# Kernel optimization log

Hardware: AMD Instinct MI355X
Metric: run time of the kernel (lower is better)

## Reference

```python
import jax, jax.numpy as jnp
import numpy as np

H = 8          # head_num
DK = 16        # qkv_dim
CLIP = 10.0    # logit clipping


def _heads(x):
    # (b, n, H*DK) -> (b, H, n, DK)
    b, n, _ = x.shape
    return x.reshape(b, n, H, DK).transpose(0, 2, 1, 3)


def setup_inputs() -> dict:
    key = jax.random.key(0)
    ks = jax.random.split(key, 10)
    batch, problem, d, klen = 2048, 100, 128, 10
    s = 1.0 / np.sqrt(d)
    problems = jax.random.uniform(ks[0], (batch, problem, 2), dtype=jnp.float32)
    encoded_nodes = jax.random.normal(ks[1], (batch, problem, d), dtype=jnp.float32)
    Wq_first = jax.random.normal(ks[2], (d, H * DK), dtype=jnp.float32) * s
    Wq_last = jax.random.normal(ks[3], (d, H * DK), dtype=jnp.float32) * s
    Wk = jax.random.normal(ks[4], (d, H * DK), dtype=jnp.float32) * s
    Wv = jax.random.normal(ks[5], (d, H * DK), dtype=jnp.float32) * s
    Wcomb = jax.random.normal(ks[6], (H * DK, d), dtype=jnp.float32) * s
    # prefix: k distinct node indices per batch row (first k of a random permutation)
    perm = jax.vmap(lambda kk: jax.random.permutation(kk, problem))(
        jax.random.split(ks[7], batch))
    prefix = perm[:, :klen].astype(jnp.int32)
    return {"problems": problems, "encoded_nodes": encoded_nodes,
            "Wq_first": Wq_first, "Wq_last": Wq_last, "Wk": Wk, "Wv": Wv,
            "Wcomb": Wcomb, "prefix": prefix}


def reference(problems, encoded_nodes, Wq_first, Wq_last, Wk, Wv, Wcomb, prefix):
    batch, problem, d = encoded_nodes.shape
    b_idx = jnp.arange(batch)
    sqrt_dk = jnp.sqrt(jnp.float32(DK))
    sqrt_d = jnp.sqrt(jnp.float32(d))

    # set_kv: precompute multi-head K, V once (single-head key = encoded_nodes)
    kh = _heads(encoded_nodes @ Wk)   # (b, H, n, DK)
    vh = _heads(encoded_nodes @ Wv)   # (b, H, n, DK)

    # set_q1: query contribution of the first node (last node of prefix)
    last0 = prefix[:, -1]
    q1 = _heads(encoded_nodes[b_idx, last0][:, None, :] @ Wq_first)  # (b, H, 1, DK)

    # visited mask from prefix
    visited0 = jnp.zeros((batch, problem), dtype=bool)
    visited0 = visited0.at[b_idx[:, None], prefix].set(True)

    def step(carry, _):
        visited, cur = carry
        enc_last = encoded_nodes[b_idx, cur][:, None, :]            # (b, 1, d)
        q = q1 + _heads(enc_last @ Wq_last)                         # (b, H, 1, DK)
        ninf = jnp.where(visited, -jnp.inf, 0.0)                    # (b, n)
        scores = jnp.einsum('bhqe,bhne->bhqn', q, kh) / sqrt_dk
        att = jax.nn.softmax(scores + ninf[:, None, None, :], axis=-1)
        mh = jnp.einsum('bhqn,bhne->bhqe', att, vh)                 # (b, H, 1, DK)
        mh = mh.transpose(0, 2, 1, 3).reshape(batch, 1, H * DK) @ Wcomb  # (b, 1, d)
        sc = jnp.einsum('bqd,bnd->bqn', mh, encoded_nodes)[:, 0] / sqrt_d  # (b, n)
        logits = CLIP * jnp.tanh(sc) + ninf
        sel = jnp.argmax(logits, axis=-1)                           # (b,)
        visited = visited.at[b_idx, sel].set(True)
        return (visited, sel), sel

    steps = problem - prefix.shape[1]
    _, sels = jax.lax.scan(step, (visited0, last0), None, length=steps)
    tour = jnp.concatenate([prefix, sels.T.astype(prefix.dtype)], axis=1)  # (b, problem)
    return tour
```

## Files before the change

### kernel.cpp

```cpp
#include <hip/hip_runtime.h>
#include <math.h>

#define N      100
#define D      128
#define KL     10
#define S0     90
#define STEPS  90
#define LDK    132
#define NT     512

__device__ __forceinline__ float dot4(float4 a, float4 b) {
  return a.x*b.x + a.y*b.y + a.z*b.z + a.w*b.w;
}
__device__ __forceinline__ void fma4(float4& acc, float a, float4 v) {
  acc.x += a*v.x; acc.y += a*v.y; acc.z += a*v.z; acc.w += a*v.w;
}

template<int RPT>
__device__ __forceinline__ void cc(const float* __restrict__ encB,
                                   const float* __restrict__ W,
                                   bool wRowMajor, int base, int cnt,
                                   const int* __restrict__ slotNode,
                                   float* __restrict__ stage, int tid) {
  const int col = tid & 127;
  const int grp = tid >> 7;
  float acc[RPT];
  int   nd [RPT];
  #pragma unroll
  for (int ii = 0; ii < RPT; ++ii) {
    acc[ii] = 0.f;
    int r = grp + 4*ii;
    nd[ii] = (r < cnt) ? __builtin_amdgcn_readfirstlane(slotNode[base + r]) : 0;
  }
  for (int dd = 0; dd < D; dd += 16) {
    float w[16];
    #pragma unroll
    for (int t = 0; t < 16; ++t)
      w[t] = wRowMajor ? W[col*D + dd + t] : W[(dd+t)*D + col];
    #pragma unroll
    for (int ii = 0; ii < RPT; ++ii) {
      int r = grp + 4*ii;
      if (r < cnt) {
        const float* er = encB + (size_t)nd[ii]*D + dd;
        float a0=0,a1=0,a2=0,a3=0;
        #pragma unroll
        for (int t = 0; t < 16; t += 4) {
          a0 += er[t]*w[t];   a1 += er[t+1]*w[t+1];
          a2 += er[t+2]*w[t+2]; a3 += er[t+3]*w[t+3];
        }
        acc[ii] += (a0+a1)+(a2+a3);
      }
    }
  }
  #pragma unroll
  for (int ii = 0; ii < RPT; ++ii) {
    int r = grp + 4*ii;
    if (r < cnt) stage[(base + r)*LDK + col] = acc[ii];
  }
}

__global__ __launch_bounds__(NT, 4)
void policy_kernel(const float* __restrict__ enc,
                   const float* __restrict__ Wq_first,
                   const float* __restrict__ Wq_last,
                   const float* __restrict__ Wk,
                   const float* __restrict__ Wv,
                   const float* __restrict__ Wcomb,
                   const int*   __restrict__ prefix,
                   int*         __restrict__ out) {
  __shared__ __align__(16) float sCE[S0*LDK];
  __shared__ __align__(16) float sq[D];
  __shared__ __align__(16) float sMh[D];
  __shared__ float sSum[8];
  __shared__ int   sSlotNode[96];
  __shared__ unsigned long long sPacked[2];
  __shared__ int   sLast0;

  const int tid = threadIdx.x;
  const int b   = blockIdx.x;
  const float* encB = enc + (size_t)b*N*D;

  if (tid < KL) out[(size_t)b*N + tid] = prefix[b*KL + tid];
  if (tid == 0) {
    unsigned vis[4] = {0u,0u,0u,0u};
    const int* pr = prefix + b*KL;
    for (int j = 0; j < KL; ++j) { int n = pr[j]; vis[n>>5] |= 1u << (n&31); }
    int cnt = 0;
    for (int n = 0; n < N; ++n)
      if (!((vis[n>>5] >> (n&31)) & 1u)) sSlotNode[cnt++] = n;
    sLast0 = pr[KL-1];
    sPacked[0] = 0ull; sPacked[1] = 0ull;
  }
  __syncthreads();

  if (tid < D) {
    const int last0 = sLast0;
    const float* er = encB + (size_t)last0*D;
    float a0=0,a1=0,a2=0,a3=0;
    #pragma unroll
    for (int d = 0; d < D; d += 4) {
      a0 += er[d]  *Wq_first[d*D     + tid];
      a1 += er[d+1]*Wq_first[(d+1)*D + tid];
      a2 += er[d+2]*Wq_first[(d+2)*D + tid];
      a3 += er[d+3]*Wq_first[(d+3)*D + tid];
    }
    sMh[tid] = (a0+a1)+(a2+a3);
  }
  __syncthreads();

  const int h = tid >> 6, l = tid & 63;

  {
    const int col = tid & 127;
    const int grp = tid >> 7;
    float acc[23]; int nd[23];
    #pragma unroll
    for (int ii = 0; ii < 23; ++ii) {
      int r = grp + 4*ii;
      acc[ii] = 0.f;
      nd[ii] = (r < S0) ? __builtin_amdgcn_readfirstlane(sSlotNode[r])
                        : ((r == S0) ? sLast0 : 0);
    }
    for (int dd = 0; dd < D; dd += 16) {
      float w[16];
      #pragma unroll
      for (int t = 0; t < 16; ++t) w[t] = Wq_last[(dd+t)*D + col];
      #pragma unroll
      for (int ii = 0; ii < 23; ++ii) {
        int r = grp + 4*ii;
        if (r <= S0) {
          const float* er = encB + (size_t)nd[ii]*D + dd;
          float a0=0,a1=0,a2=0,a3=0;
          #pragma unroll
          for (int t = 0; t < 16; t += 4) {
            a0 += er[t]*w[t];   a1 += er[t+1]*w[t+1];
            a2 += er[t+2]*w[t+2]; a3 += er[t+3]*w[t+3];
          }
          acc[ii] += (a0+a1)+(a2+a3);
        }
      }
    }
    #pragma unroll
    for (int ii = 0; ii < 23; ++ii) {
      int r = grp + 4*ii;
      if (r < S0)       sCE[r*LDK + col] = acc[ii];
      else if (r == S0) sq[col] = acc[ii] + sMh[col];
    }
  }
  __syncthreads();

  const int qcol = (h << 4) | (l & 15);
  const int qrg  = l >> 4;
  float qp[23];
  {
    const float q1c = sMh[qcol];
    #pragma unroll
    for (int ii = 0; ii < 23; ++ii) {
      int r = qrg + 4*ii;
      qp[ii] = (r < S0) ? (sCE[r*LDK + qcol] + q1c) : 0.f;
    }
  }
  __syncthreads();

  cc<23>(encB, Wk, false, 0, S0, sSlotNode, sCE, tid);
  __syncthreads();
  float4 ka0,ka1,ka2,ka3, kb0,kb1,kb2,kb3;
  {
    const float* p = &sCE[l*LDK + h*16];
    ka0 = *(const float4*)(p+0);  ka1 = *(const float4*)(p+4);
    ka2 = *(const float4*)(p+8);  ka3 = *(const float4*)(p+12);
  }
  if (l < 26) {
    const float* p = &sCE[(64+l)*LDK + h*16];
    kb0 = *(const float4*)(p+0);  kb1 = *(const float4*)(p+4);
    kb2 = *(const float4*)(p+8);  kb3 = *(const float4*)(p+12);
  } else {
    kb0=kb1=kb2=kb3 = make_float4(0.f,0.f,0.f,0.f);
  }
  __syncthreads();

  const int cQuad = tid >> 4;
  const int cStrm = tid & 15;
  const int ch    = cQuad >> 2;
  cc<12>(encB, Wv, false,  0, 48, sSlotNode, sCE, tid);
  cc<12>(encB, Wv, false, 48, 42, sSlotNode, sCE, tid);
  __syncthreads();
  float4 v0,v1,v2,v3,v4,v5;
  v0 = *(const float4*)&sCE[(cStrm     )*LDK + cQuad*4];
  v1 = *(const float4*)&sCE[(cStrm + 16)*LDK + cQuad*4];
  v2 = *(const float4*)&sCE[(cStrm + 32)*LDK + cQuad*4];
  v3 = *(const float4*)&sCE[(cStrm + 48)*LDK + cQuad*4];
  v4 = *(const float4*)&sCE[(cStrm + 64)*LDK + cQuad*4];
  v5 = (cStrm < 10) ? *(const float4*)&sCE[(cStrm + 80)*LDK + cQuad*4]
                    : make_float4(0.f,0.f,0.f,0.f);
  __syncthreads();

  cc<6>(encB, Wcomb, true,  0, 24, sSlotNode, sCE, tid);
  cc<6>(encB, Wcomb, true, 24, 24, sSlotNode, sCE, tid);
  cc<6>(encB, Wcomb, true, 48, 24, sSlotNode, sCE, tid);
  cc<6>(encB, Wcomb, true, 72, 18, sSlotNode, sCE, tid);
  __syncthreads();

  const int di  = tid >> 2;
  const int dkc = tid & 3;
  float visA = 0.f, visB = 0.f, visD = 0.f;

  for (int step = 0; step < STEPS; ++step) {
    float x0, x1;
    {
      const float4 q0 = *(const float4*)&sq[h*16 + 0];
      const float4 q1 = *(const float4*)&sq[h*16 + 4];
      const float4 q2 = *(const float4*)&sq[h*16 + 8];
      const float4 q3 = *(const float4*)&sq[h*16 + 12];
      float s0 = dot4(q0,ka0)+dot4(q1,ka1)+dot4(q2,ka2)+dot4(q3,ka3);
      x0 = expf(s0*0.25f + visA);
      x1 = 0.f;
      if (l < 26) {
        float s1 = dot4(q0,kb0)+dot4(q1,kb1)+dot4(q2,kb2)+dot4(q3,kb3);
        x1 = expf(s1*0.25f + visB);
      }
      float loc = x0 + x1;
      #pragma unroll
      for (int off = 32; off; off >>= 1) loc += __shfl_xor(loc, off);
      if (l == 0) sSum[h] = loc;
    }

    {
      const float a0 = __shfl(x0, cStrm);
      const float a1 = __shfl(x0, cStrm + 16);
      const float a2 = __shfl(x0, cStrm + 32);
      const float a3 = __shfl(x0, cStrm + 48);
      const float a4 = __shfl(x1, cStrm);
      const float a5 = __shfl(x1, cStrm + 16);
      float4 acc = make_float4(0.f,0.f,0.f,0.f);
      fma4(acc, a0, v0);
      fma4(acc, a1, v1);
      fma4(acc, a2, v2);
      fma4(acc, a3, v3);
      fma4(acc, a4, v4);
      fma4(acc, a5, v5);
      #pragma unroll
      for (int off = 1; off < 16; off <<= 1) {
        acc.x += __shfl_xor(acc.x, off);
        acc.y += __shfl_xor(acc.y, off);
        acc.z += __shfl_xor(acc.z, off);
        acc.w += __shfl_xor(acc.w, off);
      }
      if (cStrm == 0) {
        const float r = 1.0f / sSum[ch];
        float4 o; o.x=acc.x*r; o.y=acc.y*r; o.z=acc.z*r; o.w=acc.w*r;
        *(float4*)&sMh[cQuad*4] = o;
      }
    }
    __syncthreads();

    if (tid == NT-1) sPacked[(step+1)&1] = 0ull;

    if (tid < 384) {
      float a = 0.f;
      #pragma unroll
      for (int j = 0; j < 8; ++j) {
        const float4 ce = *(const float4*)&sCE[di*LDK + dkc*32 + j*4];
        const float4 mh = *(const float4*)&sMh[dkc*32 + j*4];
        a += dot4(ce, mh);
      }
      a += __shfl_xor(a, 1);
      a += __shfl_xor(a, 2);
      float val = (di < S0) ? a + visD : -INFINITY;
      int   idx = (di < S0) ? di : 127;
      #pragma unroll
      for (int off = 4; off <= 32; off <<= 1) {
        float ov = __shfl_xor(val, off);
        int   oi = __shfl_xor(idx, off);
        if (ov > val || (ov == val && oi < idx)) { val = ov; idx = oi; }
      }
      if (l == 0) {
        unsigned s = __float_as_uint(val);
        s = (s & 0x80000000u) ? ~s : (s | 0x80000000u);
        unsigned long long pk = ((unsigned long long)s << 32)
                              | (unsigned long long)(unsigned)(127 - idx);
        atomicMax(&sPacked[step&1], pk);
      }
    }
    __syncthreads();

    {
      const unsigned long long u = sPacked[step & 1];
      const int idx = __builtin_amdgcn_readfirstlane(127 - (int)(u & 0xFFull));
      if (tid == 0) out[(size_t)b*N + KL + step] = sSlotNode[idx];
      if (idx == l)      visA = -INFINITY;
      if (idx == l + 64) visB = -INFINITY;
      if (idx == di)     visD = -INFINITY;
      const int want = idx >> 2;
      float qv = qp[0];
      #pragma unroll
      for (int ii = 1; ii < 23; ++ii) qv = (want == ii) ? qp[ii] : qv;
      if (qrg == (idx & 3)) sq[qcol] = qv;
    }
  }
}

extern "C" void kernel_launch(void* const* d_in, const int* in_sizes, int n_in,
                              void* d_out, int out_size, void* d_ws, size_t ws_size,
                              hipStream_t stream) {
  const float* enc      = (const float*)d_in[1];
  const float* Wq_first = (const float*)d_in[2];
  const float* Wq_last  = (const float*)d_in[3];
  const float* Wk       = (const float*)d_in[4];
  const float* Wv       = (const float*)d_in[5];
  const float* Wcomb    = (const float*)d_in[6];
  const int*   prefix   = (const int*)d_in[7];
  const int batch = in_sizes[7] / KL;
  policy_kernel<<<batch, NT, 0, stream>>>(enc, Wq_first, Wq_last, Wk, Wv, Wcomb,
                                          prefix, (int*)d_out);
}
```

Baseline: 2.520 ms.

## Split per-node projections into a separate wide GEMM kernel via workspace

Moves the K, V, Wcomb and Wq_last projections of all 100 nodes into a separate setup kernel that uses 52 blocks per batch row and writes results to a global workspace. The decode kernel then gathers the 90 unvisited rows from the workspace into shared memory instead of computing the projections inside one 512-thread block per batch row. This exposes far more parallelism for the projection phase. In exchange it adds a round-trip of about 200 KB per batch row through global memory, computes the 10 prefix rows it does not need, and adds a second launch. It falls back to the fused kernel when the workspace is too small.

```diff
diff --git a/kernel.cpp b/kernel.cpp
--- a/kernel.cpp
+++ b/kernel.cpp
@@ -9,11 +9,77 @@
 #define LDK    132
 #define NT     512
 
+#define WS_PER_KIND 12800
+#define WS_PER_B    51200
+
 __device__ __forceinline__ float dot4(float4 a, float4 b) {
   return a.x*b.x + a.y*b.y + a.z*b.z + a.w*b.w;
 }
 __device__ __forceinline__ void fma4(float4& acc, float a, float4 v) {
   acc.x += a*v.x; acc.y += a*v.y; acc.z += a*v.z; acc.w += a*v.w;
+}
+
+__global__ __launch_bounds__(256)
+void setup_gemm(const float* __restrict__ enc,
+                const float* __restrict__ Wk,
+                const float* __restrict__ Wv,
+                const float* __restrict__ Wcomb,
+                const float* __restrict__ Wq_last,
+                float* __restrict__ ws) {
+  const int blk  = blockIdx.x;
+  const int rem  = blk % 52;
+  const int b    = blk / 52;
+  const int kind = rem / 13;
+  const int tile = rem % 13;
+  const int col  = threadIdx.x & 127;
+  const int rh   = threadIdx.x >> 7;
+  const float* W = (kind==0) ? Wk : (kind==1) ? Wv : (kind==2) ? Wcomb : Wq_last;
+  const bool rowMajor = (kind == 2);
+  const float* encB = enc + (size_t)b*N*D;
+
+  int rows[4];
+  float acc[4];
+  #pragma unroll
+  for (int j = 0; j < 4; ++j) { rows[j] = tile*8 + rh + 2*j; acc[j] = 0.f; }
+
+  for (int dd = 0; dd < D; dd += 16) {
+    float w[16];
+    #pragma unroll
+    for (int t = 0; t < 16; ++t)
+      w[t] = rowMajor ? W[col*D + dd + t] : W[(dd+t)*D + col];
+    #pragma unroll
+    for (int j = 0; j < 4; ++j) {
+      if (rows[j] < N) {
+        const float* er = encB + (size_t)rows[j]*D + dd;
+        float a0=0,a1=0,a2=0,a3=0;
+        #pragma unroll
+        for (int t = 0; t < 16; t += 4) {
+          a0 += er[t]*w[t];   a1 += er[t+1]*w[t+1];
+          a2 += er[t+2]*w[t+2]; a3 += er[t+3]*w[t+3];
+        }
+        acc[j] += (a0+a1)+(a2+a3);
+      }
+    }
+  }
+  float* o = ws + ((size_t)b*4 + kind)*WS_PER_KIND;
+  #pragma unroll
+  for (int j = 0; j < 4; ++j)
+    if (rows[j] < N) o[rows[j]*D + col] = acc[j];
+}
+
+__device__ __forceinline__ void stage90(const float* __restrict__ wsKind,
+                                        const int* __restrict__ slotNode,
+                                        float* __restrict__ sCE, int tid) {
+  const int c4  = (tid & 31) * 4;
+  const int grp = tid >> 5;
+  #pragma unroll
+  for (int ii = 0; ii < 6; ++ii) {
+    int r = grp + 16*ii;
+    if (r < S0) {
+      int nd = slotNode[r];
+      *(float4*)&sCE[r*LDK + c4] = *(const float4*)&wsKind[(size_t)nd*D + c4];
+    }
+  }
 }
 
 template<int RPT>
@@ -57,6 +123,228 @@
     int r = grp + 4*ii;
     if (r < cnt) stage[(base + r)*LDK + col] = acc[ii];
   }
+}
+
+struct DecodeState {
+  float4 ka0,ka1,ka2,ka3, kb0,kb1,kb2,kb3;
+  float4 v0,v1,v2,v3,v4,v5;
+  float  qp[23];
+};
+
+__device__ __forceinline__ void decode_loop(DecodeState& st,
+                                            float* sq, float* sMh, float* sSum,
+                                            float* sCE, int* sSlotNode,
+                                            unsigned long long* sPacked,
+                                            int tid, int b,
+                                            int* __restrict__ out) {
+  const int h = tid >> 6, l = tid & 63;
+  const int qcol = (h << 4) | (l & 15);
+  const int qrg  = l >> 4;
+  const int cQuad = tid >> 4;
+  const int cStrm = tid & 15;
+  const int ch    = cQuad >> 2;
+  const int di  = tid >> 2;
+  const int dkc = tid & 3;
+  float visA = 0.f, visB = 0.f, visD = 0.f;
+
+  for (int step = 0; step < STEPS; ++step) {
+    float x0, x1;
+    {
+      const float4 q0 = *(const float4*)&sq[h*16 + 0];
+      const float4 q1 = *(const float4*)&sq[h*16 + 4];
+      const float4 q2 = *(const float4*)&sq[h*16 + 8];
+      const float4 q3 = *(const float4*)&sq[h*16 + 12];
+      float s0 = dot4(q0,st.ka0)+dot4(q1,st.ka1)+dot4(q2,st.ka2)+dot4(q3,st.ka3);
+      x0 = expf(s0*0.25f + visA);
+      x1 = 0.f;
+      if (l < 26) {
+        float s1 = dot4(q0,st.kb0)+dot4(q1,st.kb1)+dot4(q2,st.kb2)+dot4(q3,st.kb3);
+        x1 = expf(s1*0.25f + visB);
+      }
+      float loc = x0 + x1;
+      #pragma unroll
+      for (int off = 32; off; off >>= 1) loc += __shfl_xor(loc, off);
+      if (l == 0) sSum[h] = loc;
+    }
+
+    {
+      const float a0 = __shfl(x0, cStrm);
+      const float a1 = __shfl(x0, cStrm + 16);
+      const float a2 = __shfl(x0, cStrm + 32);
+      const float a3 = __shfl(x0, cStrm + 48);
+      const float a4 = __shfl(x1, cStrm);
+      const float a5 = __shfl(x1, cStrm + 16);
+      float4 acc = make_float4(0.f,0.f,0.f,0.f);
+      fma4(acc, a0, st.v0);
+      fma4(acc, a1, st.v1);
+      fma4(acc, a2, st.v2);
+      fma4(acc, a3, st.v3);
+      fma4(acc, a4, st.v4);
+      fma4(acc, a5, st.v5);
+      #pragma unroll
+      for (int off = 1; off < 16; off <<= 1) {
+        acc.x += __shfl_xor(acc.x, off);
+        acc.y += __shfl_xor(acc.y, off);
+        acc.z += __shfl_xor(acc.z, off);
+        acc.w += __shfl_xor(acc.w, off);
+      }
+      if (cStrm == 0) {
+        const float r = 1.0f / sSum[ch];
+        float4 o; o.x=acc.x*r; o.y=acc.y*r; o.z=acc.z*r; o.w=acc.w*r;
+        *(float4*)&sMh[cQuad*4] = o;
+      }
+    }
+    __syncthreads();
+
+    if (tid == NT-1) sPacked[(step+1)&1] = 0ull;
+
+    if (tid < 384) {
+      float a = 0.f;
+      #pragma unroll
+      for (int j = 0; j < 8; ++j) {
+        const float4 ce = *(const float4*)&sCE[di*LDK + dkc*32 + j*4];
+        const float4 mh = *(const float4*)&sMh[dkc*32 + j*4];
+        a += dot4(ce, mh);
+      }
+      a += __shfl_xor(a, 1);
+      a += __shfl_xor(a, 2);
+      float val = (di < S0) ? a + visD : -INFINITY;
+      int   idx = (di < S0) ? di : 127;
+      #pragma unroll
+      for (int off = 4; off <= 32; off <<= 1) {
+        float ov = __shfl_xor(val, off);
+        int   oi = __shfl_xor(idx, off);
+        if (ov > val || (ov == val && oi < idx)) { val = ov; idx = oi; }
+      }
+      if (l == 0) {
+        unsigned s = __float_as_uint(val);
+        s = (s & 0x80000000u) ? ~s : (s | 0x80000000u);
+        unsigned long long pk = ((unsigned long long)s << 32)
+                              | (unsigned long long)(unsigned)(127 - idx);
+        atomicMax(&sPacked[step&1], pk);
+      }
+    }
+    __syncthreads();
+
+    {
+      const unsigned long long u = sPacked[step & 1];
+      const int idx = __builtin_amdgcn_readfirstlane(127 - (int)(u & 0xFFull));
+      if (tid == 0) out[(size_t)b*N + KL + step] = sSlotNode[idx];
+      if (idx == l)      visA = -INFINITY;
+      if (idx == l + 64) visB = -INFINITY;
+      if (idx == di)     visD = -INFINITY;
+      const int want = idx >> 2;
+      float qv = st.qp[0];
+      #pragma unroll
+      for (int ii = 1; ii < 23; ++ii) qv = (want == ii) ? st.qp[ii] : qv;
+      if (qrg == (idx & 3)) sq[qcol] = qv;
+    }
+  }
+}
+
+__global__ __launch_bounds__(NT, 4)
+void policy_kernel_split(const float* __restrict__ enc,
+                         const float* __restrict__ Wq_first,
+                         const int*   __restrict__ prefix,
+                         const float* __restrict__ ws,
+                         int*         __restrict__ out) {
+  __shared__ __align__(16) float sCE[S0*LDK];
+  __shared__ __align__(16) float sq[D];
+  __shared__ __align__(16) float sMh[D];
+  __shared__ float sSum[8];
+  __shared__ int   sSlotNode[96];
+  __shared__ unsigned long long sPacked[2];
+  __shared__ int   sLast0;
+
+  const int tid = threadIdx.x;
+  const int b   = blockIdx.x;
+  const float* encB = enc + (size_t)b*N*D;
+  const float* wsB  = ws + (size_t)b*WS_PER_B;
+  const float* wsK  = wsB;
+  const float* wsV  = wsB + WS_PER_KIND;
+  const float* wsCE = wsB + 2*WS_PER_KIND;
+  const float* wsQ  = wsB + 3*WS_PER_KIND;
+
+  if (tid < KL) out[(size_t)b*N + tid] = prefix[b*KL + tid];
+  if (tid == 0) {
+    unsigned vis[4] = {0u,0u,0u,0u};
+    const int* pr = prefix + b*KL;
+    for (int j = 0; j < KL; ++j) { int n = pr[j]; vis[n>>5] |= 1u << (n&31); }
+    int cnt = 0;
+    for (int n = 0; n < N; ++n)
+      if (!((vis[n>>5] >> (n&31)) & 1u)) sSlotNode[cnt++] = n;
+    sLast0 = pr[KL-1];
+    sPacked[0] = 0ull; sPacked[1] = 0ull;
+  }
+  __syncthreads();
+
+  if (tid < D) {
+    const int last0 = sLast0;
+    const float* er = encB + (size_t)last0*D;
+    float a0=0,a1=0,a2=0,a3=0;
+    #pragma unroll
+    for (int d = 0; d < D; d += 4) {
+      a0 += er[d]  *Wq_first[d*D     + tid];
+      a1 += er[d+1]*Wq_first[(d+1)*D + tid];
+      a2 += er[d+2]*Wq_first[(d+2)*D + tid];
+      a3 += er[d+3]*Wq_first[(d+3)*D + tid];
+    }
+    sMh[tid] = (a0+a1)+(a2+a3);
+  }
+  __syncthreads();
+
+  const int h = tid >> 6, l = tid & 63;
+  const int qcol = (h << 4) | (l & 15);
+  const int qrg  = l >> 4;
+  DecodeState st;
+
+  stage90(wsQ, sSlotNode, sCE, tid);
+  if (tid < D) sq[tid] = wsQ[(size_t)sLast0*D + tid] + sMh[tid];
+  __syncthreads();
+
+  {
+    const float q1c = sMh[qcol];
+    #pragma unroll
+    for (int ii = 0; ii < 23; ++ii) {
+      int r = qrg + 4*ii;
+      st.qp[ii] = (r < S0) ? (sCE[r*LDK + qcol] + q1c) : 0.f;
+    }
+  }
+  __syncthreads();
+
+  stage90(wsK, sSlotNode, sCE, tid);
+  __syncthreads();
+  {
+    const float* p = &sCE[l*LDK + h*16];
+    st.ka0 = *(const float4*)(p+0);  st.ka1 = *(const float4*)(p+4);
+    st.ka2 = *(const float4*)(p+8);  st.ka3 = *(const float4*)(p+12);
+  }
+  if (l < 26) {
+    const float* p = &sCE[(64+l)*LDK + h*16];
+    st.kb0 = *(const float4*)(p+0);  st.kb1 = *(const float4*)(p+4);
+    st.kb2 = *(const float4*)(p+8);  st.kb3 = *(const float4*)(p+12);
+  } else {
+    st.kb0=st.kb1=st.kb2=st.kb3 = make_float4(0.f,0.f,0.f,0.f);
+  }
+  __syncthreads();
+
+  const int cQuad = tid >> 4;
+  const int cStrm = tid & 15;
+  stage90(wsV, sSlotNode, sCE, tid);
+  __syncthreads();
+  st.v0 = *(const float4*)&sCE[(cStrm     )*LDK + cQuad*4];
+  st.v1 = *(const float4*)&sCE[(cStrm + 16)*LDK + cQuad*4];
+  st.v2 = *(const float4*)&sCE[(cStrm + 32)*LDK + cQuad*4];
+  st.v3 = *(const float4*)&sCE[(cStrm + 48)*LDK + cQuad*4];
+  st.v4 = *(const float4*)&sCE[(cStrm + 64)*LDK + cQuad*4];
+  st.v5 = (cStrm < 10) ? *(const float4*)&sCE[(cStrm + 80)*LDK + cQuad*4]
+                       : make_float4(0.f,0.f,0.f,0.f);
+  __syncthreads();
+
+  stage90(wsCE, sSlotNode, sCE, tid);
+  __syncthreads();
+
+  decode_loop(st, sq, sMh, sSum, sCE, sSlotNode, sPacked, tid, b, out);
 }
 
 __global__ __launch_bounds__(NT, 4)
@@ -109,6 +397,9 @@
   __syncthreads();
 
   const int h = tid >> 6, l = tid & 63;
+  const int qcol = (h << 4) | (l & 15);
+  const int qrg  = l >> 4;
+  DecodeState st;
 
   {
     const int col = tid & 127;
@@ -149,50 +440,44 @@
   }
   __syncthreads();
 
-  const int qcol = (h << 4) | (l & 15);
-  const int qrg  = l >> 4;
-  float qp[23];
   {
     const float q1c = sMh[qcol];
     #pragma unroll
     for (int ii = 0; ii < 23; ++ii) {
       int r = qrg + 4*ii;
-      qp[ii] = (r < S0) ? (sCE[r*LDK + qcol] + q1c) : 0.f;
+      st.qp[ii] = (r < S0) ? (sCE[r*LDK + qcol] + q1c) : 0.f;
     }
   }
   __syncthreads();
 
   cc<23>(encB, Wk, false, 0, S0, sSlotNode, sCE, tid);
   __syncthreads();
-  float4 ka0,ka1,ka2,ka3, kb0,kb1,kb2,kb3;
   {
     const float* p = &sCE[l*LDK + h*16];
-    ka0 = *(const float4*)(p+0);  ka1 = *(const float4*)(p+4);
-    ka2 = *(const float4*)(p+8);  ka3 = *(const float4*)(p+12);
+    st.ka0 = *(const float4*)(p+0);  st.ka1 = *(const float4*)(p+4);
+    st.ka2 = *(const float4*)(p+8);  st.ka3 = *(const float4*)(p+12);
   }
   if (l < 26) {
     const float* p = &sCE[(64+l)*LDK + h*16];
-    kb0 = *(const float4*)(p+0);  kb1 = *(const float4*)(p+4);
-    kb2 = *(const float4*)(p+8);  kb3 = *(const float4*)(p+12);
+    st.kb0 = *(const float4*)(p+0);  st.kb1 = *(const float4*)(p+4);
+    st.kb2 = *(const float4*)(p+8);  st.kb3 = *(const float4*)(p+12);
   } else {
-    kb0=kb1=kb2=kb3 = make_float4(0.f,0.f,0.f,0.f);
+    st.kb0=st.kb1=st.kb2=st.kb3 = make_float4(0.f,0.f,0.f,0.f);
   }
   __syncthreads();
 
   const int cQuad = tid >> 4;
   const int cStrm = tid & 15;
-  const int ch    = cQuad >> 2;
   cc<12>(encB, Wv, false,  0, 48, sSlotNode, sCE, tid);
   cc<12>(encB, Wv, false, 48, 42, sSlotNode, sCE, tid);
   __syncthreads();
-  float4 v0,v1,v2,v3,v4,v5;
-  v0 = *(const float4*)&sCE[(cStrm     )*LDK + cQuad*4];
-  v1 = *(const float4*)&sCE[(cStrm + 16)*LDK + cQuad*4];
-  v2 = *(const float4*)&sCE[(cStrm + 32)*LDK + cQuad*4];
-  v3 = *(const float4*)&sCE[(cStrm + 48)*LDK + cQuad*4];
-  v4 = *(const float4*)&sCE[(cStrm + 64)*LDK + cQuad*4];
-  v5 = (cStrm < 10) ? *(const float4*)&sCE[(cStrm + 80)*LDK + cQuad*4]
-                    : make_float4(0.f,0.f,0.f,0.f);
+  st.v0 = *(const float4*)&sCE[(cStrm     )*LDK + cQuad*4];
+  st.v1 = *(const float4*)&sCE[(cStrm + 16)*LDK + cQuad*4];
+  st.v2 = *(const float4*)&sCE[(cStrm + 32)*LDK + cQuad*4];
+  st.v3 = *(const float4*)&sCE[(cStrm + 48)*LDK + cQuad*4];
+  st.v4 = *(const float4*)&sCE[(cStrm + 64)*LDK + cQuad*4];
+  st.v5 = (cStrm < 10) ? *(const float4*)&sCE[(cStrm + 80)*LDK + cQuad*4]
+                       : make_float4(0.f,0.f,0.f,0.f);
   __syncthreads();
 
   cc<6>(encB, Wcomb, true,  0, 24, sSlotNode, sCE, tid);
@@ -201,103 +486,7 @@
   cc<6>(encB, Wcomb, true, 72, 18, sSlotNode, sCE, tid);
   __syncthreads();
 
-  const int di  = tid >> 2;
-  const int dkc = tid & 3;
-  float visA = 0.f, visB = 0.f, visD = 0.f;
-
-  for (int step = 0; step < STEPS; ++step) {
-    float x0, x1;
-    {
-      const float4 q0 = *(const float4*)&sq[h*16 + 0];
-      const float4 q1 = *(const float4*)&sq[h*16 + 4];
-      const float4 q2 = *(const float4*)&sq[h*16 + 8];
-      const float4 q3 = *(const float4*)&sq[h*16 + 12];
-      float s0 = dot4(q0,ka0)+dot4(q1,ka1)+dot4(q2,ka2)+dot4(q3,ka3);
-      x0 = expf(s0*0.25f + visA);
-      x1 = 0.f;
-      if (l < 26) {
-        float s1 = dot4(q0,kb0)+dot4(q1,kb1)+dot4(q2,kb2)+dot4(q3,kb3);
-        x1 = expf(s1*0.25f + visB);
-      }
-      float loc = x0 + x1;
-      #pragma unroll
-      for (int off = 32; off; off >>= 1) loc += __shfl_xor(loc, off);
-      if (l == 0) sSum[h] = loc;
-    }
-
-    {
-      const float a0 = __shfl(x0, cStrm);
-      const float a1 = __shfl(x0, cStrm + 16);
-      const float a2 = __shfl(x0, cStrm + 32);
-      const float a3 = __shfl(x0, cStrm + 48);
-      const float a4 = __shfl(x1, cStrm);
-      const float a5 = __shfl(x1, cStrm + 16);
-      float4 acc = make_float4(0.f,0.f,0.f,0.f);
-      fma4(acc, a0, v0);
-      fma4(acc, a1, v1);
-      fma4(acc, a2, v2);
-      fma4(acc, a3, v3);
-      fma4(acc, a4, v4);
-      fma4(acc, a5, v5);
-      #pragma unroll
-      for (int off = 1; off < 16; off <<= 1) {
-        acc.x += __shfl_xor(acc.x, off);
-        acc.y += __shfl_xor(acc.y, off);
-        acc.z += __shfl_xor(acc.z, off);
-        acc.w += __shfl_xor(acc.w, off);
-      }
-      if (cStrm == 0) {
-        const float r = 1.0f / sSum[ch];
-        float4 o; o.x=acc.x*r; o.y=acc.y*r; o.z=acc.z*r; o.w=acc.w*r;
-        *(float4*)&sMh[cQuad*4] = o;
-      }
-    }
-    __syncthreads();
-
-    if (tid == NT-1) sPacked[(step+1)&1] = 0ull;
-
-    if (tid < 384) {
-      float a = 0.f;
-      #pragma unroll
-      for (int j = 0; j < 8; ++j) {
-        const float4 ce = *(const float4*)&sCE[di*LDK + dkc*32 + j*4];
-        const float4 mh = *(const float4*)&sMh[dkc*32 + j*4];
-        a += dot4(ce, mh);
-      }
-      a += __shfl_xor(a, 1);
-      a += __shfl_xor(a, 2);
-      float val = (di < S0) ? a + visD : -INFINITY;
-      int   idx = (di < S0) ? di : 127;
-      #pragma unroll
-      for (int off = 4; off <= 32; off <<= 1) {
-        float ov = __shfl_xor(val, off);
-        int   oi = __shfl_xor(idx, off);
-        if (ov > val || (ov == val && oi < idx)) { val = ov; idx = oi; }
-      }
-      if (l == 0) {
-        unsigned s = __float_as_uint(val);
-        s = (s & 0x80000000u) ? ~s : (s | 0x80000000u);
-        unsigned long long pk = ((unsigned long long)s << 32)
-                              | (unsigned long long)(unsigned)(127 - idx);
-        atomicMax(&sPacked[step&1], pk);
-      }
-    }
-    __syncthreads();
-
-    {
-      const unsigned long long u = sPacked[step & 1];
-      const int idx = __builtin_amdgcn_readfirstlane(127 - (int)(u & 0xFFull));
-      if (tid == 0) out[(size_t)b*N + KL + step] = sSlotNode[idx];
-      if (idx == l)      visA = -INFINITY;
-      if (idx == l + 64) visB = -INFINITY;
-      if (idx == di)     visD = -INFINITY;
-      const int want = idx >> 2;
-      float qv = qp[0];
-      #pragma unroll
-      for (int ii = 1; ii < 23; ++ii) qv = (want == ii) ? qp[ii] : qv;
-      if (qrg == (idx & 3)) sq[qcol] = qv;
-    }
-  }
+  decode_loop(st, sq, sMh, sSum, sCE, sSlotNode, sPacked, tid, b, out);
 }
 
 extern "C" void kernel_launch(void* const* d_in, const int* in_sizes, int n_in,
@@ -311,6 +500,16 @@
   const float* Wcomb    = (const float*)d_in[6];
   const int*   prefix   = (const int*)d_in[7];
   const int batch = in_sizes[7] / KL;
-  policy_kernel<<<batch, NT, 0, stream>>>(enc, Wq_first, Wq_last, Wk, Wv, Wcomb,
-                                          prefix, (int*)d_out);
-}
+
+  const size_t need = (size_t)batch * WS_PER_B * sizeof(float);
+  if (d_ws && ws_size >= need) {
+    setup_gemm<<<batch*52, 256, 0, stream>>>(enc, Wk, Wv, Wcomb, Wq_last,
+                                             (float*)d_ws);
+    policy_kernel_split<<<batch, NT, 0, stream>>>(enc, Wq_first, prefix,
+                                                  (const float*)d_ws,
+                                                  (int*)d_out);
+  } else {
+    policy_kernel<<<batch, NT, 0, stream>>>(enc, Wq_first, Wq_last, Wk, Wv,
+                                            Wcomb, prefix, (int*)d_out);
+  }
+}
```

Result: slower. 5.849 ms (+132.1%).
